# Kernel optimization log

Hardware: AMD Instinct MI355X
Metric: run time of the kernel (lower is better)

## Reference

```python
import jax, jax.numpy as jnp
import numpy as np

EPS = 1e-5


def hyper_graph_conv(x, elements, W, b):
    """x: [B, C, N] vertex features; elements: [M, 8] vertex ids per hex element.
    Gather 8 vertex features per element, apply Linear(8C -> 8Co) on the
    concatenated features, then scatter-mean the 8 outputs back to vertices.
    Returns [B, Co, N]."""
    B, C, N = x.shape
    M = elements.shape[0]
    Co = W.shape[0] // 8
    g = x[:, :, elements]                      # [B, C, M, 8]
    g = jnp.transpose(g, (0, 2, 3, 1)).reshape(B, M, 8 * C)   # [B, M, 8C]
    h = jnp.einsum('bmk,ok->bmo', g, W) + b    # [B, M, 8Co]
    h = h.reshape(B, M * 8, Co)                # per-(element,corner) vertex outputs
    flat = elements.reshape(-1)                # [M*8]
    out = jnp.zeros((B, N, Co), dtype=x.dtype).at[:, flat, :].add(h)
    cnt = jnp.zeros((N,), dtype=x.dtype).at[flat].add(1.0)
    out = out / jnp.maximum(cnt, 1.0)[None, :, None]
    return jnp.transpose(out, (0, 2, 1))       # [B, Co, N]


def batch_norm(x, gamma, beta):
    # BatchNorm1d in training mode over [B, C, N]: stats over (B, N)
    mean = jnp.mean(x, axis=(0, 2), keepdims=True)
    var = jnp.mean(jnp.square(x - mean), axis=(0, 2), keepdims=True)
    xn = (x - mean) * jax.lax.rsqrt(var + EPS)
    return xn * gamma[None, :, None] + beta[None, :, None]


def setup_inputs() -> dict:
    key = jax.random.key(0)
    ks = jax.random.split(key, 8)
    B, Cin, Cout, N, M = 4, 8, 16, 100000, 98304
    return {
        'x': jax.random.normal(ks[0], (B, Cin, N), dtype=jnp.float32),
        'elements': jax.random.randint(ks[1], (M, 8), 0, N, dtype=jnp.int32),
        'W1': jax.random.normal(ks[2], (8 * Cout, 8 * Cin), dtype=jnp.float32) * (1.0 / np.sqrt(8 * Cin)),
        'b1': jnp.zeros((8 * Cout,), dtype=jnp.float32),
        'gamma1': jnp.ones((Cout,), dtype=jnp.float32),
        'beta1': jnp.zeros((Cout,), dtype=jnp.float32),
        'W2': jax.random.normal(ks[3], (8 * Cout, 8 * Cout), dtype=jnp.float32) * (1.0 / np.sqrt(8 * Cout)),
        'b2': jnp.zeros((8 * Cout,), dtype=jnp.float32),
        'gamma2': jnp.ones((Cout,), dtype=jnp.float32),
        'beta2': jnp.zeros((Cout,), dtype=jnp.float32),
        'Wskip': jax.random.normal(ks[4], (Cout, Cin), dtype=jnp.float32) * (1.0 / np.sqrt(Cin)),
        'bskip': jnp.zeros((Cout,), dtype=jnp.float32),
    }


def reference(x, elements, W1, b1, gamma1, beta1, W2, b2, gamma2, beta2, Wskip, bskip):
    out = hyper_graph_conv(x, elements, W1, b1)        # [B, Cout, N]
    out = jax.nn.relu(batch_norm(out, gamma1, beta1))
    out = hyper_graph_conv(out, elements, W2, b2)      # [B, Cout, N]
    out = batch_norm(out, gamma2, beta2)
    skip = jnp.einsum('bcn,oc->bon', x, Wskip) + bskip[None, :, None]  # Conv1d k=1
    out = jax.nn.relu(out + skip)
    return out
```

## Files before the change

### kernel.cpp

```cpp
#include <hip/hip_runtime.h>

#define NB 4
#define CIN 8
#define CO 16
#define NV 100000
#define NM 98304
#define NPOS (NM*8)
#define NBLK ((NV+255)/256)
#define RED_NWV 8192

typedef short s16x8 __attribute__((ext_vector_type(8)));
typedef float f32x4 __attribute__((ext_vector_type(4)));
typedef unsigned short u16;
typedef unsigned int u32;

#define OFF_CNT   0
#define OFF_NEXT  400128
#define OFF_STAT  800256
#define OFF_ROWS  800640
#define OFF_BSUM  1200768
#define OFF_POS   1202432
#define OFF_XTB   4348160
#define OFF_W1B   10748160
#define OFF_W2B   10764544
#define OFF_H1    10797312
#define OFF_ACC   23597312
#define OFF_HBUF  49197312
#define WS_NEED   149860608

static __device__ __forceinline__ u16 f2bf(float f){
  union { float f; u32 u; } v; v.f = f;
  u32 r = v.u + 0x7fffu + ((v.u >> 16) & 1u);
  return (u16)(r >> 16);
}
static __device__ __forceinline__ float bf2f_lo(u32 w){
  union { u32 u; float f; } v; v.u = w << 16; return v.f;
}
static __device__ __forceinline__ float bf2f_hi(u32 w){
  union { u32 u; float f; } v; v.u = w & 0xffff0000u; return v.f;
}
static __device__ __forceinline__ u32 pk2(float a, float b){
  return (u32)f2bf(a) | (((u32)f2bf(b)) << 16);
}

__global__ __launch_bounds__(256) void k_prep(const int* __restrict__ elem,
    const float* __restrict__ x, const float* __restrict__ W1, const float* __restrict__ W2,
    int* __restrict__ cnt, u16* __restrict__ xtb, u16* __restrict__ w1b, u16* __restrict__ w2b)
{
  __shared__ float tile[32][257];
  if (blockIdx.x < NBLK){
    int t = threadIdx.x;
    int v0 = blockIdx.x*256;
    #pragma unroll
    for (int r = 0; r < 32; r++){
      int v = v0 + t;
      tile[r][t] = (v < NV) ? x[(size_t)r*NV + v] : 0.f;
    }
    __syncthreads();
    int v = v0 + t;
    if (v < NV){
      u16 o[32] __attribute__((aligned(16)));
      #pragma unroll
      for (int r = 0; r < 32; r++) o[r] = f2bf(tile[r][t]);
      uint4* dst = (uint4*)(xtb + (size_t)v*32);
      #pragma unroll
      for (int k = 0; k < 4; k++) dst[k] = *(uint4*)(o + k*8);
    }
  } else {
    const int T1 = NPOS;
    const int T2 = T1 + 128*64;
    const int T3 = T2 + 128*128;
    int stride = (gridDim.x - NBLK)*256;
    for (int i = (blockIdx.x - NBLK)*256 + threadIdx.x; i < T3; i += stride){
      if (i < T1) { atomicAdd(cnt + elem[i], 1); }
      else if (i < T2){ int j = i - T1; w1b[j] = f2bf(W1[j]); }
      else { int j = i - T2; w2b[j] = f2bf(W2[j]); }
    }
  }
}

__global__ __launch_bounds__(256) void k_scan_a(const int* __restrict__ cnt, int* __restrict__ bsum)
{
  int v = blockIdx.x*256 + threadIdx.x;
  int x = (v < NV) ? cnt[v] : 0;
  #pragma unroll
  for (int off = 32; off > 0; off >>= 1) x += __shfl_down(x, off);
  __shared__ int ls[4];
  int wid = threadIdx.x >> 6, lane = threadIdx.x & 63;
  if (lane == 0) ls[wid] = x;
  __syncthreads();
  if (threadIdx.x == 0) bsum[blockIdx.x] = ls[0] + ls[1] + ls[2] + ls[3];
}

__global__ __launch_bounds__(256) void k_scan_c(const int* __restrict__ cnt,
    const int* __restrict__ bsum, int* __restrict__ rows)
{
  int wid = threadIdx.x >> 6, lane = threadIdx.x & 63;
  int v = blockIdx.x*256 + threadIdx.x;
  int x = (v < NV) ? cnt[v] : 0;
  int incl = x;
  #pragma unroll
  for (int off = 1; off <= 32; off <<= 1){
    int y = __shfl_up(incl, off);
    if (lane >= off) incl += y;
  }
  __shared__ int wt[4];
  __shared__ int sbase;
  if (lane == 63) wt[wid] = incl;
  if (threadIdx.x < 64){
    int s = 0;
    for (int i = threadIdx.x; i < blockIdx.x; i += 64) s += bsum[i];
    #pragma unroll
    for (int off = 32; off > 0; off >>= 1) s += __shfl_down(s, off);
    if (threadIdx.x == 0) sbase = s;
  }
  __syncthreads();
  int woff = 0;
  for (int w = 0; w < 4; w++) if (w < wid) woff += wt[w];
  if (v < NV) rows[v] = sbase + woff + incl - x;
}

__global__ __launch_bounds__(256) void k_pos(const int* __restrict__ elem,
    const int* __restrict__ rows, int* __restrict__ next, int* __restrict__ pos)
{
  int i = blockIdx.x*256 + threadIdx.x;
  if (i < NPOS){
    int v = elem[i];
    int old = atomicAdd(next + v, 1);
    pos[i] = rows[v] + old;
  }
}

__global__ __launch_bounds__(256) void k_conv1(const int* __restrict__ elem,
    const u16* __restrict__ xtb, const u16* __restrict__ w1b,
    const float* __restrict__ b1, const int* __restrict__ pos, u16* __restrict__ hbuf)
{
  const int lane = threadIdx.x & 63;
  const int col = lane & 15, kg = lane >> 4, b = lane & 3;
  s16x8 wf[8][2];
  #pragma unroll
  for (int j2 = 0; j2 < 8; j2++)
    #pragma unroll
    for (int t = 0; t < 2; t++)
      wf[j2][t] = *(const s16x8*)(w1b + (j2*16 + col)*64 + t*32 + kg*8);
  float bb[8];
  #pragma unroll
  for (int j2 = 0; j2 < 8; j2++) bb[j2] = b1[j2*16 + col];

  int wave = (int)((blockIdx.x*blockDim.x + threadIdx.x) >> 6);
  int g0 = wave, g1 = wave + 12288;
  int ma0 = g0*4 + (col >> 2), ma1 = g1*4 + (col >> 2);
  int me0 = g0*4 + kg,         me1 = g1*4 + kg;

  int e00 = elem[ma0*8 + kg], e01 = elem[ma0*8 + 4 + kg];
  int e10 = elem[ma1*8 + kg], e11 = elem[ma1*8 + 4 + kg];
  int4 p0l = *(const int4*)(pos + me0*8), p0h = *(const int4*)(pos + me0*8 + 4);
  int4 p1l = *(const int4*)(pos + me1*8), p1h = *(const int4*)(pos + me1*8 + 4);
  s16x8 a00 = *(const s16x8*)(xtb + (size_t)e00*32 + b*8);
  s16x8 a01 = *(const s16x8*)(xtb + (size_t)e01*32 + b*8);
  s16x8 a10 = *(const s16x8*)(xtb + (size_t)e10*32 + b*8);
  s16x8 a11 = *(const s16x8*)(xtb + (size_t)e11*32 + b*8);

  int pe0[8] = {p0l.x,p0l.y,p0l.z,p0l.w,p0h.x,p0h.y,p0h.z,p0h.w};
  int pe1[8] = {p1l.x,p1l.y,p1l.z,p1l.w,p1h.x,p1h.y,p1h.z,p1h.w};

  #pragma unroll
  for (int j2 = 0; j2 < 8; j2++){
    f32x4 c = {0.f,0.f,0.f,0.f};
    c = __builtin_amdgcn_mfma_f32_16x16x32_bf16(a00, wf[j2][0], c, 0, 0, 0);
    c = __builtin_amdgcn_mfma_f32_16x16x32_bf16(a01, wf[j2][1], c, 0, 0, 0);
    uint2 d; d.x = pk2(c[0]+bb[j2], c[1]+bb[j2]); d.y = pk2(c[2]+bb[j2], c[3]+bb[j2]);
    *(uint2*)(hbuf + (size_t)pe0[j2]*64 + col*4) = d;
  }
  #pragma unroll
  for (int j2 = 0; j2 < 8; j2++){
    f32x4 c = {0.f,0.f,0.f,0.f};
    c = __builtin_amdgcn_mfma_f32_16x16x32_bf16(a10, wf[j2][0], c, 0, 0, 0);
    c = __builtin_amdgcn_mfma_f32_16x16x32_bf16(a11, wf[j2][1], c, 0, 0, 0);
    uint2 d; d.x = pk2(c[0]+bb[j2], c[1]+bb[j2]); d.y = pk2(c[2]+bb[j2], c[3]+bb[j2]);
    *(uint2*)(hbuf + (size_t)pe1[j2]*64 + col*4) = d;
  }
}

__global__ __launch_bounds__(256) void k_conv2(const int* __restrict__ elem,
    const u16* __restrict__ h1, const u16* __restrict__ w2b,
    const float* __restrict__ b2, const int* __restrict__ pos, u16* __restrict__ hbuf)
{
  __shared__ u16 wl[16384];
  #pragma unroll
  for (int r = 0; r < 8; r++){
    int q = threadIdx.x + 256*r;
    int j2t = q >> 6, ln = q & 63;
    int cc = ln & 15, kk = ln >> 4;
    int j2 = j2t >> 2, tt = j2t & 3;
    *(s16x8*)(wl + (size_t)q*8) =
        *(const s16x8*)(w2b + (j2*16 + cc)*128 + tt*32 + kk*8);
  }

  const int lane = threadIdx.x & 63;
  const int col = lane & 15, kg = lane >> 4, b = lane & 3;
  const int p = kg >> 1;
  const int c0 = (kg & 1)*8;
  float bb[8];
  #pragma unroll
  for (int j2 = 0; j2 < 8; j2++) bb[j2] = b2[j2*16 + col];

  int wave = (int)((blockIdx.x*blockDim.x + threadIdx.x) >> 6);
  int g0 = wave, g1 = wave + 12288;
  int ma0 = g0*4 + (col >> 2), ma1 = g1*4 + (col >> 2);
  int me0 = g0*4 + kg,         me1 = g1*4 + kg;

  int4 e0l = *(const int4*)(elem + ma0*8), e0h = *(const int4*)(elem + ma0*8 + 4);
  int4 e1l = *(const int4*)(elem + ma1*8), e1h = *(const int4*)(elem + ma1*8 + 4);
  int4 p0l = *(const int4*)(pos + me0*8),  p0h = *(const int4*)(pos + me0*8 + 4);
  int4 p1l = *(const int4*)(pos + me1*8),  p1h = *(const int4*)(pos + me1*8 + 4);

  int v00 = p ? e0l.y : e0l.x, v01 = p ? e0l.w : e0l.z;
  int v02 = p ? e0h.y : e0h.x, v03 = p ? e0h.w : e0h.z;
  int v10 = p ? e1l.y : e1l.x, v11 = p ? e1l.w : e1l.z;
  int v12 = p ? e1h.y : e1h.x, v13 = p ? e1h.w : e1h.z;

  s16x8 af0[4], af1[4];
  af0[0] = *(const s16x8*)(h1 + (size_t)v00*64 + b*16 + c0);
  af0[1] = *(const s16x8*)(h1 + (size_t)v01*64 + b*16 + c0);
  af0[2] = *(const s16x8*)(h1 + (size_t)v02*64 + b*16 + c0);
  af0[3] = *(const s16x8*)(h1 + (size_t)v03*64 + b*16 + c0);
  af1[0] = *(const s16x8*)(h1 + (size_t)v10*64 + b*16 + c0);
  af1[1] = *(const s16x8*)(h1 + (size_t)v11*64 + b*16 + c0);
  af1[2] = *(const s16x8*)(h1 + (size_t)v12*64 + b*16 + c0);
  af1[3] = *(const s16x8*)(h1 + (size_t)v13*64 + b*16 + c0);

  int pe0[8] = {p0l.x,p0l.y,p0l.z,p0l.w,p0h.x,p0h.y,p0h.z,p0h.w};
  int pe1[8] = {p1l.x,p1l.y,p1l.z,p1l.w,p1h.x,p1h.y,p1h.z,p1h.w};

  __syncthreads();

  #pragma unroll
  for (int j2 = 0; j2 < 8; j2++){
    s16x8 w0 = *(const s16x8*)(wl + ((size_t)(j2*4 + 0)*64 + lane)*8);
    s16x8 w1 = *(const s16x8*)(wl + ((size_t)(j2*4 + 1)*64 + lane)*8);
    s16x8 w2 = *(const s16x8*)(wl + ((size_t)(j2*4 + 2)*64 + lane)*8);
    s16x8 w3 = *(const s16x8*)(wl + ((size_t)(j2*4 + 3)*64 + lane)*8);
    f32x4 c = {0.f,0.f,0.f,0.f};
    c = __builtin_amdgcn_mfma_f32_16x16x32_bf16(af0[0], w0, c, 0, 0, 0);
    c = __builtin_amdgcn_mfma_f32_16x16x32_bf16(af0[1], w1, c, 0, 0, 0);
    c = __builtin_amdgcn_mfma_f32_16x16x32_bf16(af0[2], w2, c, 0, 0, 0);
    c = __builtin_amdgcn_mfma_f32_16x16x32_bf16(af0[3], w3, c, 0, 0, 0);
    uint2 d; d.x = pk2(c[0]+bb[j2], c[1]+bb[j2]); d.y = pk2(c[2]+bb[j2], c[3]+bb[j2]);
    *(uint2*)(hbuf + (size_t)pe0[j2]*64 + col*4) = d;
  }
  #pragma unroll
  for (int j2 = 0; j2 < 8; j2++){
    s16x8 w0 = *(const s16x8*)(wl + ((size_t)(j2*4 + 0)*64 + lane)*8);
    s16x8 w1 = *(const s16x8*)(wl + ((size_t)(j2*4 + 1)*64 + lane)*8);
    s16x8 w2 = *(const s16x8*)(wl + ((size_t)(j2*4 + 2)*64 + lane)*8);
    s16x8 w3 = *(const s16x8*)(wl + ((size_t)(j2*4 + 3)*64 + lane)*8);
    f32x4 c = {0.f,0.f,0.f,0.f};
    c = __builtin_amdgcn_mfma_f32_16x16x32_bf16(af1[0], w0, c, 0, 0, 0);
    c = __builtin_amdgcn_mfma_f32_16x16x32_bf16(af1[1], w1, c, 0, 0, 0);
    c = __builtin_amdgcn_mfma_f32_16x16x32_bf16(af1[2], w2, c, 0, 0, 0);
    c = __builtin_amdgcn_mfma_f32_16x16x32_bf16(af1[3], w3, c, 0, 0, 0);
    uint2 d; d.x = pk2(c[0]+bb[j2], c[1]+bb[j2]); d.y = pk2(c[2]+bb[j2], c[3]+bb[j2]);
    *(uint2*)(hbuf + (size_t)pe1[j2]*64 + col*4) = d;
  }
}

__global__ __launch_bounds__(256) void k_reduce(const u16* __restrict__ hbuf,
    const int* __restrict__ rows, float* __restrict__ acc, float* __restrict__ stat)
{
  int lane = threadIdx.x & 63, wid = threadIdx.x >> 6;
  int k8 = lane & 7, rg = lane >> 3;
  int wv0 = (blockIdx.x*blockDim.x + threadIdx.x) >> 6;

  int vk = wv0 + lane*RED_NWV;
  int r0 = 0, r1 = 0;
  if (lane < 13 && vk < NV){
    r0 = rows[vk];
    r1 = (vk + 1 < NV) ? rows[vk + 1] : NPOS;
  }

  float st_s0 = 0.f, st_s1 = 0.f, st_q0 = 0.f, st_q1 = 0.f;

  #pragma unroll
  for (int k0 = 0; k0 < 16; k0 += 2){
    int rsA = __shfl(r0, k0),     cA = __shfl(r1, k0)     - rsA;
    int rsB = __shfl(r0, k0 + 1), cB = __shfl(r1, k0 + 1) - rsB;
    int vA = wv0 + k0*RED_NWV, vB = wv0 + (k0 + 1)*RED_NWV;

    float a0=0,a1=0,a2=0,a3=0,a4=0,a5=0,a6=0,a7=0;
    float b0=0,b1=0,b2=0,b3=0,b4=0,b5=0,b6=0,b7=0;
    const u16* pA = hbuf + (size_t)rsA*64 + lane*8;
    const u16* pB = hbuf + (size_t)rsB*64 + lane*8;
    int cm = max(cA, cB);
    for (int p = 0; p < cm; p += 8){
      uint4 dA = {0u,0u,0u,0u}, dB = {0u,0u,0u,0u};
      if (p + rg < cA) dA = *(const uint4*)(pA + (size_t)p*64);
      if (p + rg < cB) dB = *(const uint4*)(pB + (size_t)p*64);
      a0 += bf2f_lo(dA.x); a1 += bf2f_hi(dA.x); a2 += bf2f_lo(dA.y); a3 += bf2f_hi(dA.y);
      a4 += bf2f_lo(dA.z); a5 += bf2f_hi(dA.z); a6 += bf2f_lo(dA.w); a7 += bf2f_hi(dA.w);
      b0 += bf2f_lo(dB.x); b1 += bf2f_hi(dB.x); b2 += bf2f_lo(dB.y); b3 += bf2f_hi(dB.y);
      b4 += bf2f_lo(dB.z); b5 += bf2f_hi(dB.z); b6 += bf2f_lo(dB.w); b7 += bf2f_hi(dB.w);
    }
    #pragma unroll
    for (int off = 8; off <= 32; off <<= 1){
      a0 += __shfl_xor(a0, off); a1 += __shfl_xor(a1, off);
      a2 += __shfl_xor(a2, off); a3 += __shfl_xor(a3, off);
      a4 += __shfl_xor(a4, off); a5 += __shfl_xor(a5, off);
      a6 += __shfl_xor(a6, off); a7 += __shfl_xor(a7, off);
      b0 += __shfl_xor(b0, off); b1 += __shfl_xor(b1, off);
      b2 += __shfl_xor(b2, off); b3 += __shfl_xor(b3, off);
      b4 += __shfl_xor(b4, off); b5 += __shfl_xor(b5, off);
      b6 += __shfl_xor(b6, off); b7 += __shfl_xor(b7, off);
    }
    if (lane < 8){
      if (vA < NV){
        float inv = 1.0f / fmaxf((float)cA, 1.0f);
        float c0b[4] = {a0*inv, a1*inv, a2*inv, a3*inv};
        float c1b[4] = {a4*inv, a5*inv, a6*inv, a7*inv};
        #pragma unroll
        for (int q = 0; q < 4; q++){
          float2 w2; w2.x = c0b[q]; w2.y = c1b[q];
          *(float2*)(acc + ((size_t)q*NV + vA)*16 + 2*k8) = w2;
          st_s0 += c0b[q]; st_q0 += c0b[q]*c0b[q];
          st_s1 += c1b[q]; st_q1 += c1b[q]*c1b[q];
        }
      }
      if (vB < NV){
        float inv = 1.0f / fmaxf((float)cB, 1.0f);
        float c0b[4] = {b0*inv, b1*inv, b2*inv, b3*inv};
        float c1b[4] = {b4*inv, b5*inv, b6*inv, b7*inv};
        #pragma unroll
        for (int q = 0; q < 4; q++){
          float2 w2; w2.x = c0b[q]; w2.y = c1b[q];
          *(float2*)(acc + ((size_t)q*NV + vB)*16 + 2*k8) = w2;
          st_s0 += c0b[q]; st_q0 += c0b[q]*c0b[q];
          st_s1 += c1b[q]; st_q1 += c1b[q]*c1b[q];
        }
      }
    }
  }

  __shared__ float ls[4][16], lq[4][16];
  if (lane < 8){
    ls[wid][2*k8] = st_s0; ls[wid][2*k8+1] = st_s1;
    lq[wid][2*k8] = st_q0; lq[wid][2*k8+1] = st_q1;
  }
  __syncthreads();
  if (threadIdx.x < 32){
    int c2 = threadIdx.x & 15, which = threadIdx.x >> 4;
    float tot = 0.f;
    #pragma unroll
    for (int w = 0; w < 4; w++) tot += which ? lq[w][c2] : ls[w][c2];
    unsafeAtomicAdd(stat + which*16 + c2, tot);
  }
}

__global__ __launch_bounds__(256) void k_apply1(const float* __restrict__ acc,
    const float* __restrict__ stat, const float* __restrict__ gamma,
    const float* __restrict__ beta, u16* __restrict__ h1)
{
  __shared__ float sc[16], sh[16];
  if (threadIdx.x < 16){
    int co = threadIdx.x;
    const float invn = 1.0f / (float)(NB*NV);
    float m = stat[co]*invn;
    float var = stat[16+co]*invn - m*m;
    float s = gamma[co]*rsqrtf(var + 1e-5f);
    sc[co] = s; sh[co] = beta[co] - m*s;
  }
  __syncthreads();
  int idx = blockIdx.x*256 + threadIdx.x;
  int v = idx >> 2, b = idx & 3;
  if (v >= NV) return;
  const f32x4* a4 = (const f32x4*)(acc + ((size_t)b*NV + v)*16);
  u16 o[16] __attribute__((aligned(16)));
  #pragma unroll
  for (int k = 0; k < 4; k++){
    f32x4 vv = a4[k];
    #pragma unroll
    for (int t = 0; t < 4; t++){
      int co = k*4 + t;
      float val = vv[t]*sc[co] + sh[co];
      o[co] = f2bf(fmaxf(val, 0.f));
    }
  }
  uint4* dst = (uint4*)(h1 + (size_t)v*64 + b*16);
  dst[0] = *(uint4*)(o);
  dst[1] = *(uint4*)(o + 8);
}

__global__ __launch_bounds__(256) void k_final(const float* __restrict__ acc,
    const float* __restrict__ stat, const float* __restrict__ gamma,
    const float* __restrict__ beta, const float* __restrict__ x,
    const float* __restrict__ wsk, const float* __restrict__ bsk, float* __restrict__ out)
{
  __shared__ float sc[16], sh[16];
  if (threadIdx.x < 16){
    int co = threadIdx.x;
    const float invn = 1.0f / (float)(NB*NV);
    float m = stat[co]*invn;
    float var = stat[16+co]*invn - m*m;
    float s = gamma[co]*rsqrtf(var + 1e-5f);
    sc[co] = s; sh[co] = beta[co] - m*s + bsk[co];
  }
  __syncthreads();
  int n = blockIdx.x*blockDim.x + threadIdx.x;
  int b = blockIdx.y;
  if (n >= NV) return;
  float xv[8];
  #pragma unroll
  for (int c = 0; c < 8; c++) xv[c] = x[((size_t)b*8 + c)*NV + n];
  const f32x4* a4 = (const f32x4*)(acc + ((size_t)b*NV + n)*16);
  #pragma unroll
  for (int k = 0; k < 4; k++){
    f32x4 v = a4[k];
    #pragma unroll
    for (int t = 0; t < 4; t++){
      int co = k*4 + t;
      float val = v[t]*sc[co] + sh[co];
      #pragma unroll
      for (int c = 0; c < 8; c++) val += wsk[co*8+c]*xv[c];
      out[((size_t)b*16 + co)*NV + n] = fmaxf(val, 0.f);
    }
  }
}

extern "C" void kernel_launch(void* const* d_in, const int* in_sizes, int n_in,
                              void* d_out, int out_size, void* d_ws, size_t ws_size,
                              hipStream_t stream) {
  const float* x    = (const float*)d_in[0];
  const int*   elem = (const int*)  d_in[1];
  const float* W1   = (const float*)d_in[2];
  const float* b1   = (const float*)d_in[3];
  const float* g1   = (const float*)d_in[4];
  const float* be1  = (const float*)d_in[5];
  const float* W2   = (const float*)d_in[6];
  const float* b2   = (const float*)d_in[7];
  const float* g2   = (const float*)d_in[8];
  const float* be2  = (const float*)d_in[9];
  const float* Wsk  = (const float*)d_in[10];
  const float* bsk  = (const float*)d_in[11];
  float* out = (float*)d_out;

  if (ws_size < (size_t)WS_NEED) return;

  char* ws = (char*)d_ws;
  int*   cnt  = (int*)  (ws + OFF_CNT);
  int*   next = (int*)  (ws + OFF_NEXT);
  float* stat = (float*)(ws + OFF_STAT);
  int*   rows = (int*)  (ws + OFF_ROWS);
  int*   bsum = (int*)  (ws + OFF_BSUM);
  int*   pos  = (int*)  (ws + OFF_POS);
  u16*   xtb  = (u16*)  (ws + OFF_XTB);
  u16*   w1b  = (u16*)  (ws + OFF_W1B);
  u16*   w2b  = (u16*)  (ws + OFF_W2B);
  u16*   h1   = (u16*)  (ws + OFF_H1);
  float* acc  = (float*)(ws + OFF_ACC);
  u16*   hbuf = (u16*)  (ws + OFF_HBUF);

  hipMemsetAsync(ws, 0, OFF_STAT + 384, stream);

  k_prep<<<NBLK + 1024, 256, 0, stream>>>(elem, x, W1, W2, cnt, xtb, w1b, w2b);
  k_scan_a<<<NBLK, 256, 0, stream>>>(cnt, bsum);
  k_scan_c<<<NBLK, 256, 0, stream>>>(cnt, bsum, rows);
  k_pos<<<NPOS/256, 256, 0, stream>>>(elem, rows, next, pos);

  k_conv1<<<3072, 256, 0, stream>>>(elem, xtb, w1b, b1, pos, hbuf);
  k_reduce<<<2048, 256, 0, stream>>>(hbuf, rows, acc, stat);
  k_apply1<<<(NV*4 + 255)/256, 256, 0, stream>>>(acc, stat, g1, be1, h1);

  k_conv2<<<3072, 256, 0, stream>>>(elem, h1, w2b, b2, pos, hbuf);
  k_reduce<<<2048, 256, 0, stream>>>(hbuf, rows, acc, stat + 32);
  k_final<<<dim3((NV+255)/256, NB), 256, 0, stream>>>(acc, stat + 32, g2, be2, x, Wsk, bsk, out);
}
```

Measured before the change: 265.4 us.

## Restructure CSR reduce to half-wave per vertex and store means in bf16

The reduce kernel now gives each half-wave one vertex and each wave 14 contiguous vertices. It issues the first eight rows of all seven vertex pairs as upfront loads to raise memory-level parallelism, with a tail loop for vertices of higher degree. The per-vertex means are written in bf16 in a vertex-major [N][B][16] layout instead of fp32 [B][N][16], roughly halving the intermediate traffic read by the apply and final kernels. BN statistics are still summed from the fp32 values before rounding, so the normalized inputs carry a small extra bf16 rounding error.

```diff
diff --git a/kernel.cpp b/kernel.cpp
--- a/kernel.cpp
+++ b/kernel.cpp
@@ -7,7 +7,8 @@
 #define NM 98304
 #define NPOS (NM*8)
 #define NBLK ((NV+255)/256)
-#define RED_NWV 8192
+#define VPW 14
+#define REDB 1786
 
 typedef short s16x8 __attribute__((ext_vector_type(8)));
 typedef float f32x4 __attribute__((ext_vector_type(4)));
@@ -24,7 +25,7 @@
 #define OFF_W1B   10748160
 #define OFF_W2B   10764544
 #define OFF_H1    10797312
-#define OFF_ACC   23597312
+#define OFF_MBUF  23597312
 #define OFF_HBUF  49197312
 #define WS_NEED   149860608
 
@@ -266,80 +267,78 @@
 }
 
 __global__ __launch_bounds__(256) void k_reduce(const u16* __restrict__ hbuf,
-    const int* __restrict__ rows, float* __restrict__ acc, float* __restrict__ stat)
+    const int* __restrict__ rows, u16* __restrict__ mbuf, float* __restrict__ stat)
 {
   int lane = threadIdx.x & 63, wid = threadIdx.x >> 6;
-  int k8 = lane & 7, rg = lane >> 3;
-  int wv0 = (blockIdx.x*blockDim.x + threadIdx.x) >> 6;
-
-  int vk = wv0 + lane*RED_NWV;
-  int r0 = 0, r1 = 0;
-  if (lane < 13 && vk < NV){
-    r0 = rows[vk];
-    r1 = (vk + 1 < NV) ? rows[vk + 1] : NPOS;
-  }
-
-  float st_s0 = 0.f, st_s1 = 0.f, st_q0 = 0.f, st_q1 = 0.f;
-
-  #pragma unroll
-  for (int k0 = 0; k0 < 16; k0 += 2){
-    int rsA = __shfl(r0, k0),     cA = __shfl(r1, k0)     - rsA;
-    int rsB = __shfl(r0, k0 + 1), cB = __shfl(r1, k0 + 1) - rsB;
-    int vA = wv0 + k0*RED_NWV, vB = wv0 + (k0 + 1)*RED_NWV;
-
-    float a0=0,a1=0,a2=0,a3=0,a4=0,a5=0,a6=0,a7=0;
-    float b0=0,b1=0,b2=0,b3=0,b4=0,b5=0,b6=0,b7=0;
-    const u16* pA = hbuf + (size_t)rsA*64 + lane*8;
-    const u16* pB = hbuf + (size_t)rsB*64 + lane*8;
-    int cm = max(cA, cB);
-    for (int p = 0; p < cm; p += 8){
-      uint4 dA = {0u,0u,0u,0u}, dB = {0u,0u,0u,0u};
-      if (p + rg < cA) dA = *(const uint4*)(pA + (size_t)p*64);
-      if (p + rg < cB) dB = *(const uint4*)(pB + (size_t)p*64);
-      a0 += bf2f_lo(dA.x); a1 += bf2f_hi(dA.x); a2 += bf2f_lo(dA.y); a3 += bf2f_hi(dA.y);
-      a4 += bf2f_lo(dA.z); a5 += bf2f_hi(dA.z); a6 += bf2f_lo(dA.w); a7 += bf2f_hi(dA.w);
-      b0 += bf2f_lo(dB.x); b1 += bf2f_hi(dB.x); b2 += bf2f_lo(dB.y); b3 += bf2f_hi(dB.y);
-      b4 += bf2f_lo(dB.z); b5 += bf2f_hi(dB.z); b6 += bf2f_lo(dB.w); b7 += bf2f_hi(dB.w);
-    }
-    #pragma unroll
-    for (int off = 8; off <= 32; off <<= 1){
+  int half = lane >> 5;
+  int hl   = lane & 31;
+  int k8   = lane & 7;
+  int rg   = (lane >> 3) & 3;
+  int w = (blockIdx.x*blockDim.x + threadIdx.x) >> 6;
+  int v0 = w * VPW;
+
+  int vv = v0 + lane;
+  int rr = 0;
+  if (lane < VPW + 1) rr = (vv < NV) ? rows[vv] : NPOS;
+
+  int rs[7], ce[7];
+  #pragma unroll
+  for (int j = 0; j < 7; j++){
+    rs[j] = __shfl(rr, 2*j + half);
+    ce[j] = __shfl(rr, 2*j + half + 1) - rs[j];
+  }
+
+  uint4 d0[7], d1[7];
+  #pragma unroll
+  for (int j = 0; j < 7; j++){
+    uint4 z = {0u,0u,0u,0u};
+    d0[j] = z; d1[j] = z;
+    const u16* base = hbuf + (size_t)rs[j]*64 + hl*8;
+    if (rg     < ce[j]) d0[j] = *(const uint4*)(base);
+    if (4 + rg < ce[j]) d1[j] = *(const uint4*)(base + 4*64);
+  }
+
+  float st_s0 = 0.f, st_q0 = 0.f, st_s1 = 0.f, st_q1 = 0.f;
+
+  #pragma unroll
+  for (int j = 0; j < 7; j++){
+    float a0,a1,a2,a3,a4,a5,a6,a7;
+    {
+      uint4 dA = d0[j], dB = d1[j];
+      a0 = bf2f_lo(dA.x)+bf2f_lo(dB.x); a1 = bf2f_hi(dA.x)+bf2f_hi(dB.x);
+      a2 = bf2f_lo(dA.y)+bf2f_lo(dB.y); a3 = bf2f_hi(dA.y)+bf2f_hi(dB.y);
+      a4 = bf2f_lo(dA.z)+bf2f_lo(dB.z); a5 = bf2f_hi(dA.z)+bf2f_hi(dB.z);
+      a6 = bf2f_lo(dA.w)+bf2f_lo(dB.w); a7 = bf2f_hi(dA.w)+bf2f_hi(dB.w);
+    }
+    for (int p = 8; p < ce[j]; p += 4){
+      uint4 d = {0u,0u,0u,0u};
+      if (p + rg < ce[j]) d = *(const uint4*)(hbuf + (size_t)(rs[j]+p)*64 + hl*8);
+      a0 += bf2f_lo(d.x); a1 += bf2f_hi(d.x); a2 += bf2f_lo(d.y); a3 += bf2f_hi(d.y);
+      a4 += bf2f_lo(d.z); a5 += bf2f_hi(d.z); a6 += bf2f_lo(d.w); a7 += bf2f_hi(d.w);
+    }
+    #pragma unroll
+    for (int off = 8; off <= 16; off <<= 1){
       a0 += __shfl_xor(a0, off); a1 += __shfl_xor(a1, off);
       a2 += __shfl_xor(a2, off); a3 += __shfl_xor(a3, off);
       a4 += __shfl_xor(a4, off); a5 += __shfl_xor(a5, off);
       a6 += __shfl_xor(a6, off); a7 += __shfl_xor(a7, off);
-      b0 += __shfl_xor(b0, off); b1 += __shfl_xor(b1, off);
-      b2 += __shfl_xor(b2, off); b3 += __shfl_xor(b3, off);
-      b4 += __shfl_xor(b4, off); b5 += __shfl_xor(b5, off);
-      b6 += __shfl_xor(b6, off); b7 += __shfl_xor(b7, off);
-    }
-    if (lane < 8){
-      if (vA < NV){
-        float inv = 1.0f / fmaxf((float)cA, 1.0f);
-        float c0b[4] = {a0*inv, a1*inv, a2*inv, a3*inv};
-        float c1b[4] = {a4*inv, a5*inv, a6*inv, a7*inv};
-        #pragma unroll
-        for (int q = 0; q < 4; q++){
-          float2 w2; w2.x = c0b[q]; w2.y = c1b[q];
-          *(float2*)(acc + ((size_t)q*NV + vA)*16 + 2*k8) = w2;
-          st_s0 += c0b[q]; st_q0 += c0b[q]*c0b[q];
-          st_s1 += c1b[q]; st_q1 += c1b[q]*c1b[q];
-        }
+    }
+    int v = v0 + 2*j + half;
+    if (hl < 8 && v < NV){
+      float inv = 1.0f / fmaxf((float)ce[j], 1.0f);
+      float c0b[4] = {a0*inv, a1*inv, a2*inv, a3*inv};
+      float c1b[4] = {a4*inv, a5*inv, a6*inv, a7*inv};
+      #pragma unroll
+      for (int q = 0; q < 4; q++){
+        *(u32*)(mbuf + (size_t)v*64 + q*16 + 2*k8) = pk2(c0b[q], c1b[q]);
+        st_s0 += c0b[q]; st_q0 += c0b[q]*c0b[q];
+        st_s1 += c1b[q]; st_q1 += c1b[q]*c1b[q];
       }
-      if (vB < NV){
-        float inv = 1.0f / fmaxf((float)cB, 1.0f);
-        float c0b[4] = {b0*inv, b1*inv, b2*inv, b3*inv};
-        float c1b[4] = {b4*inv, b5*inv, b6*inv, b7*inv};
-        #pragma unroll
-        for (int q = 0; q < 4; q++){
-          float2 w2; w2.x = c0b[q]; w2.y = c1b[q];
-          *(float2*)(acc + ((size_t)q*NV + vB)*16 + 2*k8) = w2;
-          st_s0 += c0b[q]; st_q0 += c0b[q]*c0b[q];
-          st_s1 += c1b[q]; st_q1 += c1b[q]*c1b[q];
-        }
-      }
-    }
-  }
-
+    }
+  }
+
+  st_s0 += __shfl_xor(st_s0, 32); st_q0 += __shfl_xor(st_q0, 32);
+  st_s1 += __shfl_xor(st_s1, 32); st_q1 += __shfl_xor(st_q1, 32);
   __shared__ float ls[4][16], lq[4][16];
   if (lane < 8){
     ls[wid][2*k8] = st_s0; ls[wid][2*k8+1] = st_s1;
@@ -350,12 +349,12 @@
     int c2 = threadIdx.x & 15, which = threadIdx.x >> 4;
     float tot = 0.f;
     #pragma unroll
-    for (int w = 0; w < 4; w++) tot += which ? lq[w][c2] : ls[w][c2];
+    for (int w2 = 0; w2 < 4; w2++) tot += which ? lq[w2][c2] : ls[w2][c2];
     unsafeAtomicAdd(stat + which*16 + c2, tot);
   }
 }
 
-__global__ __launch_bounds__(256) void k_apply1(const float* __restrict__ acc,
+__global__ __launch_bounds__(256) void k_apply1(const u16* __restrict__ mbuf,
     const float* __restrict__ stat, const float* __restrict__ gamma,
     const float* __restrict__ beta, u16* __restrict__ h1)
 {
@@ -372,24 +371,24 @@
   int idx = blockIdx.x*256 + threadIdx.x;
   int v = idx >> 2, b = idx & 3;
   if (v >= NV) return;
-  const f32x4* a4 = (const f32x4*)(acc + ((size_t)b*NV + v)*16);
+  const uint4* src = (const uint4*)(mbuf + (size_t)v*64 + b*16);
+  uint4 m0 = src[0], m1 = src[1];
+  u32 mw[8] = {m0.x,m0.y,m0.z,m0.w,m1.x,m1.y,m1.z,m1.w};
   u16 o[16] __attribute__((aligned(16)));
   #pragma unroll
-  for (int k = 0; k < 4; k++){
-    f32x4 vv = a4[k];
-    #pragma unroll
-    for (int t = 0; t < 4; t++){
-      int co = k*4 + t;
-      float val = vv[t]*sc[co] + sh[co];
-      o[co] = f2bf(fmaxf(val, 0.f));
-    }
+  for (int k = 0; k < 8; k++){
+    int c0 = 2*k, c1 = 2*k + 1;
+    float va = bf2f_lo(mw[k])*sc[c0] + sh[c0];
+    float vb = bf2f_hi(mw[k])*sc[c1] + sh[c1];
+    o[c0] = f2bf(fmaxf(va, 0.f));
+    o[c1] = f2bf(fmaxf(vb, 0.f));
   }
   uint4* dst = (uint4*)(h1 + (size_t)v*64 + b*16);
   dst[0] = *(uint4*)(o);
   dst[1] = *(uint4*)(o + 8);
 }
 
-__global__ __launch_bounds__(256) void k_final(const float* __restrict__ acc,
+__global__ __launch_bounds__(256) void k_final(const u16* __restrict__ mbuf,
     const float* __restrict__ stat, const float* __restrict__ gamma,
     const float* __restrict__ beta, const float* __restrict__ x,
     const float* __restrict__ wsk, const float* __restrict__ bsk, float* __restrict__ out)
@@ -410,14 +409,15 @@
   float xv[8];
   #pragma unroll
   for (int c = 0; c < 8; c++) xv[c] = x[((size_t)b*8 + c)*NV + n];
-  const f32x4* a4 = (const f32x4*)(acc + ((size_t)b*NV + n)*16);
-  #pragma unroll
-  for (int k = 0; k < 4; k++){
-    f32x4 v = a4[k];
-    #pragma unroll
-    for (int t = 0; t < 4; t++){
-      int co = k*4 + t;
-      float val = v[t]*sc[co] + sh[co];
+  const uint4* src = (const uint4*)(mbuf + (size_t)n*64 + b*16);
+  uint4 m0 = src[0], m1 = src[1];
+  u32 mw[8] = {m0.x,m0.y,m0.z,m0.w,m1.x,m1.y,m1.z,m1.w};
+  #pragma unroll
+  for (int k = 0; k < 8; k++){
+    #pragma unroll
+    for (int h = 0; h < 2; h++){
+      int co = 2*k + h;
+      float val = (h ? bf2f_hi(mw[k]) : bf2f_lo(mw[k]))*sc[co] + sh[co];
       #pragma unroll
       for (int c = 0; c < 8; c++) val += wsk[co*8+c]*xv[c];
       out[((size_t)b*16 + co)*NV + n] = fmaxf(val, 0.f);
@@ -455,7 +455,7 @@
   u16*   w1b  = (u16*)  (ws + OFF_W1B);
   u16*   w2b  = (u16*)  (ws + OFF_W2B);
   u16*   h1   = (u16*)  (ws + OFF_H1);
-  float* acc  = (float*)(ws + OFF_ACC);
+  u16*   mbuf = (u16*)  (ws + OFF_MBUF);
   u16*   hbuf = (u16*)  (ws + OFF_HBUF);
 
   hipMemsetAsync(ws, 0, OFF_STAT + 384, stream);
@@ -466,10 +466,10 @@
   k_pos<<<NPOS/256, 256, 0, stream>>>(elem, rows, next, pos);
 
   k_conv1<<<3072, 256, 0, stream>>>(elem, xtb, w1b, b1, pos, hbuf);
-  k_reduce<<<2048, 256, 0, stream>>>(hbuf, rows, acc, stat);
-  k_apply1<<<(NV*4 + 255)/256, 256, 0, stream>>>(acc, stat, g1, be1, h1);
+  k_reduce<<<REDB, 256, 0, stream>>>(hbuf, rows, mbuf, stat);
+  k_apply1<<<(NV*4 + 255)/256, 256, 0, stream>>>(mbuf, stat, g1, be1, h1);
 
   k_conv2<<<3072, 256, 0, stream>>>(elem, h1, w2b, b2, pos, hbuf);
-  k_reduce<<<2048, 256, 0, stream>>>(hbuf, rows, acc, stat + 32);
-  k_final<<<dim3((NV+255)/256, NB), 256, 0, stream>>>(acc, stat + 32, g2, be2, x, Wsk, bsk, out);
-}
+  k_reduce<<<REDB, 256, 0, stream>>>(hbuf, rows, mbuf, stat + 32);
+  k_final<<<dim3((NV+255)/256, NB), 256, 0, stream>>>(mbuf, stat + 32, g2, be2, x, Wsk, bsk, out);
+}
```

Result: faster. 259.6 us (-2.2%).
